# Kernel tuning notes

Hardware: AMD Instinct MI355X
Metric: run time of the kernel (lower is better)

The kernel has to match this reference:

```python
import jax, jax.numpy as jnp
import numpy as np

EMB = 1024
HEADS = 16
S = EMB // HEADS  # per-head dim


def setup_inputs() -> dict:
    key = jax.random.key(0)
    ks = jax.random.split(key, 6)
    x = jax.random.normal(ks[0], (4, 2048, EMB), dtype=jnp.float32)
    # torch nn.Linear(s, s, bias=False): weight [out, in], y = x @ W.T
    Wk = jax.random.normal(ks[1], (S, S), dtype=jnp.float32) * (1.0 / np.sqrt(S))
    Wq = jax.random.normal(ks[2], (S, S), dtype=jnp.float32) * (1.0 / np.sqrt(S))
    Wv = jax.random.normal(ks[3], (S, S), dtype=jnp.float32) * (1.0 / np.sqrt(S))
    # unifyHeads: Linear(heads*s, emb) with bias
    Wu = jax.random.normal(ks[4], (EMB, EMB), dtype=jnp.float32) * (1.0 / np.sqrt(EMB))
    bu = jax.random.normal(ks[5], (EMB,), dtype=jnp.float32) * 0.01
    return {"x": x, "Wk": Wk, "Wq": Wq, "Wv": Wv, "Wu": Wu, "bu": bu}


def reference(x, Wk, Wq, Wv, Wu, bu):
    b, t, e = x.shape
    h, s = HEADS, S
    x4 = x.reshape(b, t, h, s)
    # per-head narrow projections (y = x @ W.T)
    k = jnp.einsum('bths,os->bhto', x4, Wk)  # [b,h,t,s]
    q = jnp.einsum('bths,os->bhto', x4, Wq)
    v = jnp.einsum('bths,os->bhto', x4, Wv)
    scale = e ** 0.25
    q = q / scale
    k = k / scale
    dot = jnp.einsum('bhqs,bhks->bhqk', q, k)  # [b,h,t,t]
    attn = jax.nn.softmax(dot, axis=-1)
    out = jnp.einsum('bhqk,bhks->bhqs', attn, v)  # [b,h,t,s]
    out = out.transpose(0, 2, 1, 3).reshape(b, t, h * s)
    return out @ Wu.T + bu
```

## Files before the change

### kernel.cpp

```cpp
#include <hip/hip_runtime.h>
#include <hip/hip_bf16.h>

#define BB 4
#define TT 2048
#define HH 16
#define SS 64
#define EE 1024

typedef __attribute__((ext_vector_type(8))) short short8;
typedef __attribute__((ext_vector_type(4))) short short4v;
typedef __attribute__((ext_vector_type(4))) float float4v;

__device__ inline short f2bf(float f) {
    union { __hip_bfloat16 h; short s; } u;
    u.h = __float2bfloat16(f);
    return u.s;
}

__device__ inline unsigned pack_bf(float lo, float hi) {
    return ((unsigned)(unsigned short)f2bf(hi) << 16) | (unsigned short)f2bf(lo);
}

__device__ inline float4v mfma16(short8 a, short8 b, float4v c) {
    return __builtin_amdgcn_mfma_f32_16x16x32_bf16(a, b, c, 0, 0, 0);
}

#define LDSP(p) ((__attribute__((address_space(3))) void*)(p))
#define GLBP(p) ((const __attribute__((address_space(1))) void*)(p))

__global__ __launch_bounds__(256) void k_qkv(
    const float* __restrict__ x, const float* __restrict__ Wk,
    const float* __restrict__ Wq, const float* __restrict__ Wv,
    short* __restrict__ qb, short* __restrict__ kb, short* __restrict__ vb)
{
    __shared__ __attribute__((aligned(16))) short lw[3][64][72];
    const int tid = threadIdx.x;
    const float pscale = 0.17677669529663687f;

    for (int i = 0; i < 12; i++) {
        int u = tid + 256 * i;
        int w = u >> 10;
        int rem = u & 1023;
        int row = rem >> 4;
        int col = (rem & 15) * 4;
        const float* Wp = (w == 0) ? Wk : ((w == 1) ? Wq : Wv);
        float4v f = *reinterpret_cast<const float4v*>(Wp + row * 64 + col);
        float sc = (w == 2) ? 1.0f : pscale;
        short4v s4;
        s4.x = f2bf(f.x * sc); s4.y = f2bf(f.y * sc);
        s4.z = f2bf(f.z * sc); s4.w = f2bf(f.w * sc);
        *reinterpret_cast<short4v*>(&lw[w][row][col]) = s4;
    }
    __syncthreads();

    const int wave = tid >> 6, lane = tid & 63;
    const int quad = lane >> 4, m = lane & 15;
    const long r0 = (long)blockIdx.x * 64 + wave * 16;
    const int bt = (int)(r0 >> 4);
    const int b = bt >> 11, t = bt & 2047;

    const float* xrow = x + (r0 + m) * 64;
    short8 af[2];
    for (int ks = 0; ks < 2; ks++) {
        float4v f0 = *reinterpret_cast<const float4v*>(xrow + ks * 32 + quad * 8);
        float4v f1 = *reinterpret_cast<const float4v*>(xrow + ks * 32 + quad * 8 + 4);
        short8 a;
        a[0] = f2bf(f0.x); a[1] = f2bf(f0.y); a[2] = f2bf(f0.z); a[3] = f2bf(f0.w);
        a[4] = f2bf(f1.x); a[5] = f2bf(f1.y); a[6] = f2bf(f1.z); a[7] = f2bf(f1.w);
        af[ks] = a;
    }

    for (int w = 0; w < 3; w++) {
        short* dst = (w == 0) ? kb : ((w == 1) ? qb : vb);
        for (int c = 0; c < 4; c++) {
            float4v acc = {0.f, 0.f, 0.f, 0.f};
            for (int ks = 0; ks < 2; ks++) {
                short8 bf = *reinterpret_cast<const short8*>(&lw[w][c * 16 + m][ks * 32 + quad * 8]);
                acc = mfma16(af[ks], bf, acc);
            }
            for (int r = 0; r < 4; r++) {
                int h = quad * 4 + r;
                long di = (((long)(b * 16 + h) * 2048) + t) * 64 + c * 16 + m;
                dst[di] = f2bf(acc[r]);
            }
        }
    }
}

__global__ __launch_bounds__(256) void k_prep(
    const short* __restrict__ vb, short* __restrict__ vtb,
    const float* __restrict__ Wu, short* __restrict__ wub)
{
    __shared__ short lt[64][65];
    const int bid = blockIdx.x;
    const int tid = threadIdx.x;
    if (bid < 2048) {
        int bh = bid >> 5, tb = bid & 31;
        const short* src = vb + ((long)bh * 2048 + tb * 64) * 64;
        for (int i = 0; i < 2; i++) {
            int u = tid + 256 * i;
            int row = u >> 3, seg = u & 7;
            short8 d = *reinterpret_cast<const short8*>(src + row * 64 + seg * 8);
            for (int j = 0; j < 8; j++) lt[seg * 8 + j][row] = d[j];
        }
        __syncthreads();
        short* dst = vtb + (long)bh * 64 * 2048 + tb * 64;
        for (int i = 0; i < 2; i++) {
            int u = tid + 256 * i;
            int srow = u >> 3, seg = u & 7;
            short8 d;
            for (int j = 0; j < 8; j++) d[j] = lt[srow][seg * 8 + j];
            *reinterpret_cast<short8*>(dst + (long)srow * 2048 + seg * 8) = d;
        }
    } else {
        int cb = bid - 2048;
        long base = (long)cb * 4096;
        for (int i = 0; i < 4; i++) {
            long e = base + (long)tid * 4 + (long)i * 1024;
            float4v f = *reinterpret_cast<const float4v*>(Wu + e);
            short4v s;
            s.x = f2bf(f.x); s.y = f2bf(f.y); s.z = f2bf(f.z); s.w = f2bf(f.w);
            *reinterpret_cast<short4v*>(wub + e) = s;
        }
    }
}

__global__ __launch_bounds__(256, 2) void k_attn(
    const short* __restrict__ qb, const short* __restrict__ kb,
    const short* __restrict__ vtb, short* __restrict__ ob)
{
    __shared__ __attribute__((aligned(16))) short kt_s[4096];
    __shared__ __attribute__((aligned(16))) short vt_s[4096];

    const int tid = threadIdx.x;
    const int wave = tid >> 6, lane = tid & 63;
    const int quad = lane >> 4, m = lane & 15;
    const int qblk = blockIdx.x, bh = blockIdx.y;
    const int q0 = qblk * 256;
    const long qoff = (long)bh * 2048 * 64;

    const short* kbase = kb + qoff;
    const short* vtbase = vtb + (long)bh * 64 * 2048;

    short8 qf[4][2];
    for (int sub = 0; sub < 4; sub++) {
        const short* qrow = qb + qoff + (long)(q0 + wave * 64 + sub * 16 + m) * 64;
        qf[sub][0] = *reinterpret_cast<const short8*>(qrow + quad * 8);
        qf[sub][1] = *reinterpret_cast<const short8*>(qrow + 32 + quad * 8);
    }

    float l[4] = {0.f, 0.f, 0.f, 0.f};
    float4v oacc[4][4];
    for (int s = 0; s < 4; s++)
        for (int c = 0; c < 4; c++) oacc[s][c] = (float4v){0.f, 0.f, 0.f, 0.f};

    for (int kt = 0; kt < 32; kt++) {
        for (int i = 0; i < 2; i++) {
            int u = i * 256 + tid;
            int row = u >> 3;
            int cb = (u & 7) ^ (row & 7);
            const short* gp = kbase + (long)(kt * 64 + row) * 64 + cb * 8;
            short* lp = kt_s + (i * 256 + wave * 64) * 8;
            __builtin_amdgcn_global_load_lds(GLBP(gp), LDSP(lp), 16, 0, 0);
        }
        for (int i = 0; i < 2; i++) {
            int g = i * 256 + tid;
            int d = g >> 3, a = g & 7;
            union { short8 v; unsigned long long u[2]; } uv;
            uv.v = *reinterpret_cast<const short8*>(vtbase + (long)d * 2048 + kt * 64 + a * 8);
            for (int h = 0; h < 2; h++) {
                int key0 = a * 8 + 4 * h;
                int c = key0 >> 4, qk = (key0 >> 2) & 3;
                int kk = (c >> 1) * 32 + qk * 8 + (c & 1) * 4;
                int idx = d * 64 + (((kk >> 3) ^ (d & 7)) * 8) + (kk & 7);
                *reinterpret_cast<unsigned long long*>(vt_s + idx) = uv.u[h];
            }
        }
        __syncthreads();

        short8 kf[4][2], vfr[4][2];
        for (int c = 0; c < 4; c++)
            for (int ks = 0; ks < 2; ks++)
                kf[c][ks] = *reinterpret_cast<const short8*>(
                    kt_s + (c * 16 + m) * 64 + (((ks * 4 + quad) ^ (m & 7)) * 8));
        for (int c2 = 0; c2 < 4; c2++)
            for (int ks = 0; ks < 2; ks++)
                vfr[c2][ks] = *reinterpret_cast<const short8*>(
                    vt_s + (c2 * 16 + m) * 64 + (((ks * 4 + quad) ^ (m & 7)) * 8));

        for (int sub = 0; sub < 4; sub++) {
            float4v st[4];
            for (int c = 0; c < 4; c++) {
                float4v z = {0.f, 0.f, 0.f, 0.f};
                z = mfma16(kf[c][0], qf[sub][0], z);
                z = mfma16(kf[c][1], qf[sub][1], z);
                st[c] = z;
            }
            __attribute__((aligned(16))) unsigned pp[8];
            float ls = 0.f;
            for (int c = 0; c < 4; c++) {
                float e0 = __expf(st[c][0]);
                float e1 = __expf(st[c][1]);
                float e2 = __expf(st[c][2]);
                float e3 = __expf(st[c][3]);
                ls += (e0 + e1) + (e2 + e3);
                pp[c * 2]     = pack_bf(e0, e1);
                pp[c * 2 + 1] = pack_bf(e2, e3);
            }
            l[sub] += ls;
            const short8* pf = reinterpret_cast<const short8*>(pp);
            for (int ks = 0; ks < 2; ks++)
                for (int c2 = 0; c2 < 4; c2++)
                    oacc[sub][c2] = mfma16(vfr[c2][ks], pf[ks], oacc[sub][c2]);
        }
        __syncthreads();
    }

    const int b = bh >> 4, h = bh & 15;
    for (int sub = 0; sub < 4; sub++) {
        float lv = l[sub];
        lv += __shfl_xor(lv, 16);
        lv += __shfl_xor(lv, 32);
        float li = 1.0f / lv;
        int t = q0 + wave * 64 + sub * 16 + m;
        long rowbase = (((long)(b * 2048 + t)) * 16 + h) * 64;
        for (int c2 = 0; c2 < 4; c2++) {
            unsigned w0 = pack_bf(oacc[sub][c2][0] * li, oacc[sub][c2][1] * li);
            unsigned w1 = pack_bf(oacc[sub][c2][2] * li, oacc[sub][c2][3] * li);
            unsigned long long wq = (unsigned long long)w0 | ((unsigned long long)w1 << 32);
            *reinterpret_cast<unsigned long long*>(ob + rowbase + c2 * 16 + quad * 4) = wq;
        }
    }
}

__global__ __launch_bounds__(256) void k_out(
    const short* __restrict__ ob, const short* __restrict__ wub,
    const float* __restrict__ bu, float* __restrict__ y)
{
    __shared__ __attribute__((aligned(16))) short a_s[128][72];
    __shared__ __attribute__((aligned(16))) short b_s[128][72];

    const int tid = threadIdx.x;
    const int wave = tid >> 6, lane = tid & 63;
    const int quad = lane >> 4, m = lane & 15;
    const int nb = blockIdx.x, mb = blockIdx.y;
    const long mbase = (long)mb * 128;
    const int nbase = nb * 128;
    const int wm = (wave & 1) * 64, wn = (wave >> 1) * 64;

    float4v acc[4][4];
    for (int i = 0; i < 4; i++)
        for (int j = 0; j < 4; j++) acc[i][j] = (float4v){0.f, 0.f, 0.f, 0.f};

    for (int kt = 0; kt < 16; kt++) {
        for (int i = 0; i < 4; i++) {
            int u = tid + 256 * i;
            int row = u >> 3, seg = u & 7;
            *reinterpret_cast<short8*>(&a_s[row][seg * 8]) =
                *reinterpret_cast<const short8*>(ob + (mbase + row) * 1024 + kt * 64 + seg * 8);
            *reinterpret_cast<short8*>(&b_s[row][seg * 8]) =
                *reinterpret_cast<const short8*>(wub + (long)(nbase + row) * 1024 + kt * 64 + seg * 8);
        }
        __syncthreads();
        for (int ks = 0; ks < 2; ks++) {
            short8 af[4], bf[4];
            for (int i = 0; i < 4; i++)
                af[i] = *reinterpret_cast<const short8*>(&a_s[wm + i * 16 + m][ks * 32 + quad * 8]);
            for (int j = 0; j < 4; j++)
                bf[j] = *reinterpret_cast<const short8*>(&b_s[wn + j * 16 + m][ks * 32 + quad * 8]);
            for (int i = 0; i < 4; i++)
                for (int j = 0; j < 4; j++)
                    acc[i][j] = mfma16(af[i], bf[j], acc[i][j]);
        }
        __syncthreads();
    }

    for (int j = 0; j < 4; j++) {
        int o = nbase + wn + j * 16 + m;
        float bias = bu[o];
        for (int i = 0; i < 4; i++) {
            for (int r = 0; r < 4; r++) {
                long row = mbase + wm + i * 16 + quad * 4 + r;
                y[row * 1024 + o] = acc[i][j][r] + bias;
            }
        }
    }
}

extern "C" void kernel_launch(void* const* d_in, const int* in_sizes, int n_in,
                              void* d_out, int out_size, void* d_ws, size_t ws_size,
                              hipStream_t stream)
{
    const float* x  = (const float*)d_in[0];
    const float* Wk = (const float*)d_in[1];
    const float* Wq = (const float*)d_in[2];
    const float* Wv = (const float*)d_in[3];
    const float* Wu = (const float*)d_in[4];
    const float* bu = (const float*)d_in[5];
    float* y = (float*)d_out;

    char* ws = (char*)d_ws;
    const size_t SEG = 16777216;
    short* qb  = (short*)(ws);
    short* kb  = (short*)(ws + 1 * SEG);
    short* vb  = (short*)(ws + 2 * SEG);
    short* vtb = (short*)(ws + 3 * SEG);
    short* ob  = (short*)(ws + 4 * SEG);
    short* wub = (short*)(ws + 5 * SEG);

    hipLaunchKernelGGL(k_qkv, dim3(2048), dim3(256), 0, stream, x, Wk, Wq, Wv, qb, kb, vb);
    hipLaunchKernelGGL(k_prep, dim3(2304), dim3(256), 0, stream, vb, vtb, Wu, wub);
    hipLaunchKernelGGL(k_attn, dim3(8, 64), dim3(256), 0, stream, qb, kb, vtb, ob);
    hipLaunchKernelGGL(k_out, dim3(8, 64), dim3(256), 0, stream, ob, wub, bu, y);
}
```

Measured before the change: 223.8 us.

## Double-buffer attention tiles, use exp2 with folded scale, MFMA row sums, async GEMM loads

New measurement: 211.8 us. 1.06x faster.

```diff
diff --git a/kernel.cpp b/kernel.cpp
--- a/kernel.cpp
+++ b/kernel.cpp
@@ -10,6 +10,7 @@
 typedef __attribute__((ext_vector_type(8))) short short8;
 typedef __attribute__((ext_vector_type(4))) short short4v;
 typedef __attribute__((ext_vector_type(4))) float float4v;
+typedef unsigned long long ull;
 
 __device__ inline short f2bf(float f) {
     union { __hip_bfloat16 h; short s; } u;
@@ -21,6 +22,12 @@
     return ((unsigned)(unsigned short)f2bf(hi) << 16) | (unsigned short)f2bf(lo);
 }
 
+__device__ inline unsigned pack_trunc(float lo, float hi) {
+    unsigned a = __builtin_bit_cast(unsigned, lo);
+    unsigned b = __builtin_bit_cast(unsigned, hi);
+    return (b & 0xFFFF0000u) | (a >> 16);
+}
+
 __device__ inline float4v mfma16(short8 a, short8 b, float4v c) {
     return __builtin_amdgcn_mfma_f32_16x16x32_bf16(a, b, c, 0, 0, 0);
 }
@@ -35,7 +42,7 @@
 {
     __shared__ __attribute__((aligned(16))) short lw[3][64][72];
     const int tid = threadIdx.x;
-    const float pscale = 0.17677669529663687f;
+    const float sq = 0.21233045f;
 
     for (int i = 0; i < 12; i++) {
         int u = tid + 256 * i;
@@ -45,7 +52,7 @@
         int col = (rem & 15) * 4;
         const float* Wp = (w == 0) ? Wk : ((w == 1) ? Wq : Wv);
         float4v f = *reinterpret_cast<const float4v*>(Wp + row * 64 + col);
-        float sc = (w == 2) ? 1.0f : pscale;
+        float sc = (w == 2) ? 1.0f : sq;
         short4v s4;
         s4.x = f2bf(f.x * sc); s4.y = f2bf(f.y * sc);
         s4.z = f2bf(f.z * sc); s4.w = f2bf(f.w * sc);
@@ -70,19 +77,19 @@
         af[ks] = a;
     }
 
+    const long tb = ((long)(b * 16 + m) * 2048 + t) * 64;
     for (int w = 0; w < 3; w++) {
         short* dst = (w == 0) ? kb : ((w == 1) ? qb : vb);
         for (int c = 0; c < 4; c++) {
             float4v acc = {0.f, 0.f, 0.f, 0.f};
             for (int ks = 0; ks < 2; ks++) {
-                short8 bf = *reinterpret_cast<const short8*>(&lw[w][c * 16 + m][ks * 32 + quad * 8]);
-                acc = mfma16(af[ks], bf, acc);
-            }
-            for (int r = 0; r < 4; r++) {
-                int h = quad * 4 + r;
-                long di = (((long)(b * 16 + h) * 2048) + t) * 64 + c * 16 + m;
-                dst[di] = f2bf(acc[r]);
-            }
+                short8 wf = *reinterpret_cast<const short8*>(&lw[w][c * 16 + m][ks * 32 + quad * 8]);
+                acc = mfma16(wf, af[ks], acc);
+            }
+            unsigned lo = pack_bf(acc[0], acc[1]);
+            unsigned hi = pack_bf(acc[2], acc[3]);
+            ull wq = (ull)lo | ((ull)hi << 32);
+            *reinterpret_cast<ull*>(dst + tb + c * 16 + quad * 4) = wq;
         }
     }
 }
@@ -129,8 +136,8 @@
     const short* __restrict__ qb, const short* __restrict__ kb,
     const short* __restrict__ vtb, short* __restrict__ ob)
 {
-    __shared__ __attribute__((aligned(16))) short kt_s[4096];
-    __shared__ __attribute__((aligned(16))) short vt_s[4096];
+    __shared__ __attribute__((aligned(16))) short kt_s[2][4096];
+    __shared__ __attribute__((aligned(16))) short vt_s[2][4096];
 
     const int tid = threadIdx.x;
     const int wave = tid >> 6, lane = tid & 63;
@@ -149,44 +156,69 @@
         qf[sub][1] = *reinterpret_cast<const short8*>(qrow + 32 + quad * 8);
     }
 
-    float l[4] = {0.f, 0.f, 0.f, 0.f};
+    const short8 ones = (short8)((short)0x3F80);
+
     float4v oacc[4][4];
-    for (int s = 0; s < 4; s++)
+    float4v lacc[4];
+    for (int s = 0; s < 4; s++) {
+        lacc[s] = (float4v){0.f, 0.f, 0.f, 0.f};
         for (int c = 0; c < 4; c++) oacc[s][c] = (float4v){0.f, 0.f, 0.f, 0.f};
-
+    }
+
+    for (int i = 0; i < 2; i++) {
+        int u = i * 256 + tid;
+        int row = u >> 3;
+        int cb = (u & 7) ^ (row & 7);
+        const short* gp = kbase + (long)row * 64 + cb * 8;
+        short* lp = &kt_s[0][(i * 256 + wave * 64) * 8];
+        __builtin_amdgcn_global_load_lds(GLBP(gp), LDSP(lp), 16, 0, 0);
+    }
+    for (int i = 0; i < 2; i++) {
+        int g = i * 256 + tid;
+        int d = g >> 3, a = g & 7;
+        union { short8 v; ull u[2]; } uv;
+        uv.v = *reinterpret_cast<const short8*>(vtbase + (long)d * 2048 + a * 8);
+        for (int h = 0; h < 2; h++) {
+            int key0 = a * 8 + 4 * h;
+            int c = key0 >> 4, qk = (key0 >> 2) & 3;
+            int kk = (c >> 1) * 32 + qk * 8 + (c & 1) * 4;
+            int idx = d * 64 + (((kk >> 3) ^ (d & 7)) * 8) + (kk & 7);
+            *reinterpret_cast<ull*>(&vt_s[0][idx]) = uv.u[h];
+        }
+    }
+
+    int p = 0;
     for (int kt = 0; kt < 32; kt++) {
-        for (int i = 0; i < 2; i++) {
-            int u = i * 256 + tid;
-            int row = u >> 3;
-            int cb = (u & 7) ^ (row & 7);
-            const short* gp = kbase + (long)(kt * 64 + row) * 64 + cb * 8;
-            short* lp = kt_s + (i * 256 + wave * 64) * 8;
-            __builtin_amdgcn_global_load_lds(GLBP(gp), LDSP(lp), 16, 0, 0);
-        }
-        for (int i = 0; i < 2; i++) {
-            int g = i * 256 + tid;
-            int d = g >> 3, a = g & 7;
-            union { short8 v; unsigned long long u[2]; } uv;
-            uv.v = *reinterpret_cast<const short8*>(vtbase + (long)d * 2048 + kt * 64 + a * 8);
-            for (int h = 0; h < 2; h++) {
-                int key0 = a * 8 + 4 * h;
-                int c = key0 >> 4, qk = (key0 >> 2) & 3;
-                int kk = (c >> 1) * 32 + qk * 8 + (c & 1) * 4;
-                int idx = d * 64 + (((kk >> 3) ^ (d & 7)) * 8) + (kk & 7);
-                *reinterpret_cast<unsigned long long*>(vt_s + idx) = uv.u[h];
-            }
-        }
         __syncthreads();
+
+        const bool pref = (kt < 31);
+        union { short8 v; ull u[2]; } vreg[2];
+        if (pref) {
+            for (int i = 0; i < 2; i++) {
+                int u = i * 256 + tid;
+                int row = u >> 3;
+                int cb = (u & 7) ^ (row & 7);
+                const short* gp = kbase + (long)((kt + 1) * 64 + row) * 64 + cb * 8;
+                short* lp = &kt_s[p ^ 1][(i * 256 + wave * 64) * 8];
+                __builtin_amdgcn_global_load_lds(GLBP(gp), LDSP(lp), 16, 0, 0);
+            }
+            for (int i = 0; i < 2; i++) {
+                int g = i * 256 + tid;
+                int d = g >> 3, a = g & 7;
+                vreg[i].v = *reinterpret_cast<const short8*>(
+                    vtbase + (long)d * 2048 + (kt + 1) * 64 + a * 8);
+            }
+        }
 
         short8 kf[4][2], vfr[4][2];
         for (int c = 0; c < 4; c++)
             for (int ks = 0; ks < 2; ks++)
                 kf[c][ks] = *reinterpret_cast<const short8*>(
-                    kt_s + (c * 16 + m) * 64 + (((ks * 4 + quad) ^ (m & 7)) * 8));
+                    &kt_s[p][(c * 16 + m) * 64 + (((ks * 4 + quad) ^ (m & 7)) * 8)]);
         for (int c2 = 0; c2 < 4; c2++)
             for (int ks = 0; ks < 2; ks++)
                 vfr[c2][ks] = *reinterpret_cast<const short8*>(
-                    vt_s + (c2 * 16 + m) * 64 + (((ks * 4 + quad) ^ (m & 7)) * 8));
+                    &vt_s[p][(c2 * 16 + m) * 64 + (((ks * 4 + quad) ^ (m & 7)) * 8)]);
 
         for (int sub = 0; sub < 4; sub++) {
             float4v st[4];
@@ -197,38 +229,48 @@
                 st[c] = z;
             }
             __attribute__((aligned(16))) unsigned pp[8];
-            float ls = 0.f;
             for (int c = 0; c < 4; c++) {
-                float e0 = __expf(st[c][0]);
-                float e1 = __expf(st[c][1]);
-                float e2 = __expf(st[c][2]);
-                float e3 = __expf(st[c][3]);
-                ls += (e0 + e1) + (e2 + e3);
-                pp[c * 2]     = pack_bf(e0, e1);
-                pp[c * 2 + 1] = pack_bf(e2, e3);
-            }
-            l[sub] += ls;
+                float e0 = __builtin_amdgcn_exp2f(st[c][0]);
+                float e1 = __builtin_amdgcn_exp2f(st[c][1]);
+                float e2 = __builtin_amdgcn_exp2f(st[c][2]);
+                float e3 = __builtin_amdgcn_exp2f(st[c][3]);
+                pp[c * 2]     = pack_trunc(e0, e1);
+                pp[c * 2 + 1] = pack_trunc(e2, e3);
+            }
             const short8* pf = reinterpret_cast<const short8*>(pp);
+            lacc[sub] = mfma16(ones, pf[0], lacc[sub]);
+            lacc[sub] = mfma16(ones, pf[1], lacc[sub]);
             for (int ks = 0; ks < 2; ks++)
                 for (int c2 = 0; c2 < 4; c2++)
                     oacc[sub][c2] = mfma16(vfr[c2][ks], pf[ks], oacc[sub][c2]);
         }
-        __syncthreads();
+
+        if (pref) {
+            for (int i = 0; i < 2; i++) {
+                int g = i * 256 + tid;
+                int d = g >> 3, a = g & 7;
+                for (int h = 0; h < 2; h++) {
+                    int key0 = a * 8 + 4 * h;
+                    int c = key0 >> 4, qk = (key0 >> 2) & 3;
+                    int kk = (c >> 1) * 32 + qk * 8 + (c & 1) * 4;
+                    int idx = d * 64 + (((kk >> 3) ^ (d & 7)) * 8) + (kk & 7);
+                    *reinterpret_cast<ull*>(&vt_s[p ^ 1][idx]) = vreg[i].u[h];
+                }
+            }
+        }
+        p ^= 1;
     }
 
     const int b = bh >> 4, h = bh & 15;
     for (int sub = 0; sub < 4; sub++) {
-        float lv = l[sub];
-        lv += __shfl_xor(lv, 16);
-        lv += __shfl_xor(lv, 32);
-        float li = 1.0f / lv;
+        float li = 1.0f / lacc[sub][0];
         int t = q0 + wave * 64 + sub * 16 + m;
         long rowbase = (((long)(b * 2048 + t)) * 16 + h) * 64;
         for (int c2 = 0; c2 < 4; c2++) {
             unsigned w0 = pack_bf(oacc[sub][c2][0] * li, oacc[sub][c2][1] * li);
             unsigned w1 = pack_bf(oacc[sub][c2][2] * li, oacc[sub][c2][3] * li);
-            unsigned long long wq = (unsigned long long)w0 | ((unsigned long long)w1 << 32);
-            *reinterpret_cast<unsigned long long*>(ob + rowbase + c2 * 16 + quad * 4) = wq;
+            ull wq = (ull)w0 | ((ull)w1 << 32);
+            *reinterpret_cast<ull*>(ob + rowbase + c2 * 16 + quad * 4) = wq;
         }
     }
 }
@@ -237,8 +279,8 @@
     const short* __restrict__ ob, const short* __restrict__ wub,
     const float* __restrict__ bu, float* __restrict__ y)
 {
-    __shared__ __attribute__((aligned(16))) short a_s[128][72];
-    __shared__ __attribute__((aligned(16))) short b_s[128][72];
+    __shared__ __attribute__((aligned(16))) short a_s[8192];
+    __shared__ __attribute__((aligned(16))) short b_s[8192];
 
     const int tid = threadIdx.x;
     const int wave = tid >> 6, lane = tid & 63;
@@ -254,20 +296,25 @@
 
     for (int kt = 0; kt < 16; kt++) {
         for (int i = 0; i < 4; i++) {
-            int u = tid + 256 * i;
-            int row = u >> 3, seg = u & 7;
-            *reinterpret_cast<short8*>(&a_s[row][seg * 8]) =
-                *reinterpret_cast<const short8*>(ob + (mbase + row) * 1024 + kt * 64 + seg * 8);
-            *reinterpret_cast<short8*>(&b_s[row][seg * 8]) =
-                *reinterpret_cast<const short8*>(wub + (long)(nbase + row) * 1024 + kt * 64 + seg * 8);
+            int u = i * 256 + tid;
+            int row = u >> 3;
+            int c = (u & 7) ^ (row & 7);
+            const short* gpA = ob + (mbase + row) * 1024 + kt * 64 + c * 8;
+            const short* gpB = wub + (long)(nbase + row) * 1024 + kt * 64 + c * 8;
+            short* lpA = a_s + (i * 256 + wave * 64) * 8;
+            short* lpB = b_s + (i * 256 + wave * 64) * 8;
+            __builtin_amdgcn_global_load_lds(GLBP(gpA), LDSP(lpA), 16, 0, 0);
+            __builtin_amdgcn_global_load_lds(GLBP(gpB), LDSP(lpB), 16, 0, 0);
         }
         __syncthreads();
         for (int ks = 0; ks < 2; ks++) {
             short8 af[4], bf[4];
             for (int i = 0; i < 4; i++)
-                af[i] = *reinterpret_cast<const short8*>(&a_s[wm + i * 16 + m][ks * 32 + quad * 8]);
+                af[i] = *reinterpret_cast<const short8*>(
+                    a_s + (wm + i * 16 + m) * 64 + (((ks * 4 + quad) ^ (m & 7)) * 8));
             for (int j = 0; j < 4; j++)
-                bf[j] = *reinterpret_cast<const short8*>(&b_s[wn + j * 16 + m][ks * 32 + quad * 8]);
+                bf[j] = *reinterpret_cast<const short8*>(
+                    b_s + (wn + j * 16 + m) * 64 + (((ks * 4 + quad) ^ (m & 7)) * 8));
             for (int i = 0; i < 4; i++)
                 for (int j = 0; j < 4; j++)
                     acc[i][j] = mfma16(af[i], bf[j], acc[i][j]);
```
